# Performance work log

Hardware: AMD Instinct MI355X
Metric: run time of the kernel (lower is better)

## Reference

```python
import jax, jax.numpy as jnp
import numpy as np

EMBED = 1024
HEADS = 16
HEAD_DIM = EMBED // HEADS
OUT = 1024


def setup_inputs() -> dict:
    key = jax.random.key(0)
    ks = jax.random.split(key, 6)
    x = jax.random.normal(ks[0], (4, 2048, EMBED), dtype=jnp.float32)
    # per-head projection weights, torch Linear convention: [out_features, in_features]
    s = 1.0 / np.sqrt(HEAD_DIM)
    Wv = jax.random.uniform(ks[1], (HEAD_DIM, HEAD_DIM), jnp.float32, -s, s)
    Wk = jax.random.uniform(ks[2], (HEAD_DIM, HEAD_DIM), jnp.float32, -s, s)
    Wq = jax.random.uniform(ks[3], (HEAD_DIM, HEAD_DIM), jnp.float32, -s, s)
    so = 1.0 / np.sqrt(EMBED)
    Wo = jax.random.uniform(ks[4], (OUT, EMBED), jnp.float32, -so, so)
    bo = jax.random.uniform(ks[5], (OUT,), jnp.float32, -so, so)
    return {"x": x, "Wq": Wq, "Wk": Wk, "Wv": Wv, "Wo": Wo, "bo": bo}


def reference(x, Wq, Wk, Wv, Wo, bo):
    N, L, _ = x.shape
    xh = x.reshape(N, L, HEADS, HEAD_DIM)  # nqhd
    q = jnp.einsum('nqhd,ed->nqhe', xh, Wq)
    k = jnp.einsum('nkhd,ed->nkhe', xh, Wk)
    v = jnp.einsum('nkhd,ed->nkhe', xh, Wv)
    # full score matrix [N, H, Q, K], scaled by sqrt(embed_size) as in source
    energy = jnp.einsum('nqhd,nkhd->nhqk', q, k) / np.sqrt(EMBED).astype(np.float32)
    attn = jax.nn.softmax(energy, axis=3)
    out = jnp.einsum('nhqk,nkhd->nqhd', attn, v).reshape(N, L, EMBED)
    return out @ Wo.T + bo
```

## Files before the change

kernel.cpp:

```cpp
#include <hip/hip_runtime.h>
#include <hip/hip_bf16.h>
#include <stdint.h>
#include <stddef.h>


typedef __attribute__((ext_vector_type(8))) short bf16x8;
typedef __attribute__((ext_vector_type(4))) float f32x4;
typedef __attribute__((ext_vector_type(4))) short short4v;
typedef __attribute__((ext_vector_type(2))) uint32_t uint2v;

__device__ __forceinline__ f32x4 mfma16(bf16x8 a, bf16x8 b, f32x4 c) {
    return __builtin_amdgcn_mfma_f32_16x16x32_bf16(a, b, c, 0, 0, 0);
}

__device__ __forceinline__ short f2bf(float x) {
    union { float f; uint32_t u; } v; v.f = x;
    uint32_t r = (v.u + 0x7FFFu + ((v.u >> 16) & 1u)) >> 16;
    return (short)(uint16_t)r;
}

__device__ __forceinline__ uint32_t pk2bf(float a, float b) {
    union { __hip_bfloat162 h; uint32_t u; } v;
    v.h = __float22bfloat162_rn(float2{a, b});
    return v.u;
}

__device__ __forceinline__ bf16x8 cvt8(const float* __restrict__ p) {
    f32x4 a = *(const f32x4*)p;
    f32x4 b = *(const f32x4*)(p + 4);
    bf16x8 r;
    r[0] = f2bf(a[0]); r[1] = f2bf(a[1]); r[2] = f2bf(a[2]); r[3] = f2bf(a[3]);
    r[4] = f2bf(b[0]); r[5] = f2bf(b[1]); r[6] = f2bf(b[2]); r[7] = f2bf(b[3]);
    return r;
}

__device__ __forceinline__ void swap16(uint32_t a, uint32_t b,
                                       uint32_t& lo, uint32_t& hi) {
#if __has_builtin(__builtin_amdgcn_permlane16_swap)
    uint2v r = __builtin_amdgcn_permlane16_swap(a, b, false, false);
    lo = r[0]; hi = r[1];
#else
    int lane = (int)(threadIdx.x & 63);
    uint32_t bl = (uint32_t)__shfl((int)b, lane & 47);
    uint32_t ah = (uint32_t)__shfl((int)a, lane | 16);
    lo = (lane & 16) ? bl : a;
    hi = (lane & 16) ? b : ah;
#endif
}

__global__ __launch_bounds__(256)
void wpack_kernel(const float* __restrict__ Wo, const float* __restrict__ Wq,
                  const float* __restrict__ Wk, const float* __restrict__ Wv,
                  short* __restrict__ wo_f, short* __restrict__ wqkv_f) {
    int b = blockIdx.x;
    if (b < 512) {
        int idx = b * 256 + threadIdx.x;
        int nrow = idx >> 7;
        int k0 = (idx & 127) * 8;
        bf16x8 v = cvt8(Wo + (size_t)nrow * 1024 + k0);
        int ntile = nrow >> 4, lcn = nrow & 15;
        int kseg = k0 >> 5, qd = (k0 >> 3) & 3;
        *(bf16x8*)(wo_f + ((size_t)(ntile * 32 + kseg) * 64 + qd * 16 + lcn) * 8) = v;
    } else {
        const float* W = (b == 512) ? Wq : (b == 513) ? Wk : Wv;
        short* dst = wqkv_f + (size_t)(b - 512) * 4096;
        for (int u = threadIdx.x; u < 512; u += 256) {
            int seg = u >> 6, ln = u & 63;
            int nt = seg >> 1, kf = seg & 1, lq = ln >> 4, lcn = ln & 15;
            bf16x8 v = cvt8(W + (nt * 16 + lcn) * 64 + kf * 32 + lq * 8);
            *(bf16x8*)(dst + u * 8) = v;
        }
    }
}

__global__ __launch_bounds__(256)
void kvproj_kernel(const float* __restrict__ x, const short* __restrict__ wqkv_f,
                   short* __restrict__ kf_ws, short* __restrict__ vf_ws) {
    __shared__ alignas(16) short kbuf[128 * 72];
    __shared__ alignas(16) short vbuf[64 * 136];
    int tid = threadIdx.x;
    int lt = blockIdx.x & 15, nh = blockIdx.x >> 4;
    int n = nh >> 4, h = nh & 15;
    int l0 = lt * 128, kt0 = lt * 2;
    int wv = tid >> 6, lane = tid & 63, quad = lane >> 4, lc = lane & 15;
    const short* wkf = wqkv_f + 4096 + lane * 8;
    const short* wvf = wqkv_f + 8192 + lane * 8;

    for (int u = tid; u < 1024; u += 256) {
        int r = u >> 3, c = (u & 7) * 8;
        *(bf16x8*)(kbuf + r * 72 + c) =
            cvt8(x + (size_t)(n * 2048 + l0 + r) * 1024 + h * 64 + c);
    }
    __syncthreads();

    bf16x8 xa[2][2];
    for (int mt = 0; mt < 2; ++mt)
        for (int kf = 0; kf < 2; ++kf)
            xa[mt][kf] = *(bf16x8*)(kbuf + (wv * 32 + mt * 16 + lc) * 72 + kf * 32 + quad * 8);

    f32x4 ka[2][4] = {}, va[2][4] = {};
    for (int nt = 0; nt < 4; ++nt)
        for (int kf = 0; kf < 2; ++kf) {
            bf16x8 wkb = *(const bf16x8*)(wkf + (nt * 2 + kf) * 512);
            bf16x8 wvb = *(const bf16x8*)(wvf + (nt * 2 + kf) * 512);
            for (int mt = 0; mt < 2; ++mt) {
                ka[mt][nt] = mfma16(xa[mt][kf], wkb, ka[mt][nt]);
                va[mt][nt] = mfma16(xa[mt][kf], wvb, va[mt][nt]);
            }
        }

    for (int mt = 0; mt < 2; ++mt) {
        int off = wv * 32 + mt * 16;
        for (int nt = 0; nt < 4; ++nt) {
            short4v pv;
            for (int i = 0; i < 4; ++i) {
                kbuf[(off + quad * 4 + i) * 72 + nt * 16 + lc] = f2bf(ka[mt][nt][i]);
                pv[i] = f2bf(va[mt][nt][i]);
            }
            *(short4v*)(vbuf + (nt * 16 + lc) * 136 + off + quad * 4) = pv;
        }
    }
    __syncthreads();

    size_t base = (size_t)nh * 131072 + (size_t)kt0 * 4096;
    for (int u = tid; u < 1024; u += 256) {
        int tile = u >> 9, rem = u & 511, seg = rem >> 6, ln = u & 63;
        int t = seg >> 1, kf = seg & 1;
        int lq = ln >> 4, ll = ln & 15;
        int bq = ((lq & 1) << 1) | (lq >> 1);
        bf16x8 kw = *(bf16x8*)(kbuf + (tile * 64 + t * 16 + ll) * 72 + kf * 32 + lq * 8);
        *(bf16x8*)(kf_ws + base + (size_t)tile * 4096 + seg * 512 + ln * 8) = kw;
        bf16x8 vw = *(bf16x8*)(vbuf + (t * 16 + ll) * 136 + tile * 64 + kf * 32 + bq * 8);
        *(bf16x8*)(vf_ws + base + (size_t)tile * 4096 + seg * 512 + ln * 8) = vw;
    }
}

__global__ __launch_bounds__(256, 2)
void flash_kernel(const float* __restrict__ x, const short* __restrict__ wqkv_f,
                  const short* __restrict__ kf_ws, const short* __restrict__ vf_ws,
                  short* __restrict__ ao) {
    __shared__ alignas(16) short pbuf[256 * 72];
    int tid = threadIdx.x;
    int nh = blockIdx.x & 63, qt = blockIdx.x >> 6;
    int n = nh >> 4, h = nh & 15;
    int q0 = qt * 256;
    int wv = tid >> 6, lane = tid & 63, quad = lane >> 4, lc = lane & 15;

    for (int u = tid; u < 2048; u += 256) {
        int r = u >> 3, c = (u & 7) * 8;
        *(bf16x8*)(pbuf + r * 72 + c) =
            cvt8(x + (size_t)(n * 2048 + q0 + r) * 1024 + h * 64 + c);
    }
    __syncthreads();
    {
        const short* wqf = wqkv_f + lane * 8;
        bf16x8 xa[4][2];
        for (int mt = 0; mt < 4; ++mt)
            for (int kf = 0; kf < 2; ++kf)
                xa[mt][kf] = *(bf16x8*)(pbuf + (wv * 64 + mt * 16 + lc) * 72 +
                                        kf * 32 + quad * 8);
        f32x4 qacc[4][4] = {};
        for (int nt = 0; nt < 4; ++nt)
            for (int kf = 0; kf < 2; ++kf) {
                bf16x8 wb = *(const bf16x8*)(wqf + (nt * 2 + kf) * 512);
                for (int mt = 0; mt < 4; ++mt)
                    qacc[mt][nt] = mfma16(xa[mt][kf], wb, qacc[mt][nt]);
            }
        const float QS = 0.04508422002778011f;
        for (int mt = 0; mt < 4; ++mt)
            for (int nt = 0; nt < 4; ++nt)
                for (int i = 0; i < 4; ++i)
                    pbuf[(wv * 64 + mt * 16 + quad * 4 + i) * 72 + nt * 16 + lc] =
                        f2bf(qacc[mt][nt][i] * QS);
    }
    __syncthreads();
    bf16x8 qa[4][2];
    for (int mt = 0; mt < 4; ++mt)
        for (int kf = 0; kf < 2; ++kf)
            qa[mt][kf] = *(bf16x8*)(pbuf + (wv * 64 + mt * 16 + lc) * 72 +
                                    kf * 32 + quad * 8);

    f32x4 o[4][4] = {};
    float lsum[4] = {0.f, 0.f, 0.f, 0.f};
    const short* kbase = kf_ws + (size_t)nh * 131072 + lane * 8;
    const short* vbase = vf_ws + (size_t)nh * 131072 + lane * 8;

    for (int kt = 0; kt < 32; ++kt) {
        const short* kp = kbase + (size_t)kt * 4096;
        const short* vp = vbase + (size_t)kt * 4096;
        bf16x8 kA[4][2], vA[4][2];
#pragma unroll
        for (int t = 0; t < 4; ++t)
            for (int kf = 0; kf < 2; ++kf) {
                kA[t][kf] = *(const bf16x8*)(kp + (t * 2 + kf) * 512);
                vA[t][kf] = *(const bf16x8*)(vp + (t * 2 + kf) * 512);
            }

#pragma unroll
        for (int q2 = 0; q2 < 4; ++q2) {
            f32x4 s[4];
#pragma unroll
            for (int t = 0; t < 4; ++t) {
                f32x4 acc = {};
                acc = mfma16(kA[t][0], qa[q2][0], acc);
                acc = mfma16(kA[t][1], qa[q2][1], acc);
                s[t] = acc;
            }
            uint32_t p0[4], p1[4];
            float ts = 0.f;
#pragma unroll
            for (int t = 0; t < 4; ++t) {
                float e0 = __builtin_amdgcn_exp2f(s[t][0]);
                float e1 = __builtin_amdgcn_exp2f(s[t][1]);
                float e2 = __builtin_amdgcn_exp2f(s[t][2]);
                float e3 = __builtin_amdgcn_exp2f(s[t][3]);
                ts += (e0 + e1) + (e2 + e3);
                p0[t] = pk2bf(e0, e1);
                p1[t] = pk2bf(e2, e3);
            }
            lsum[q2] += ts;
#pragma unroll
            for (int kf = 0; kf < 2; ++kf) {
                uint32_t r0, r1, r2, r3;
                swap16(p0[2 * kf], p0[2 * kf + 1], r0, r2);
                swap16(p1[2 * kf], p1[2 * kf + 1], r1, r3);
                union { uint32_t u[4]; bf16x8 v; } fr;
                fr.u[0] = r0; fr.u[1] = r1; fr.u[2] = r2; fr.u[3] = r3;
#pragma unroll
                for (int dt = 0; dt < 4; ++dt)
                    o[q2][dt] = mfma16(vA[dt][kf], fr.v, o[q2][dt]);
            }
        }
    }

    for (int q2 = 0; q2 < 4; ++q2) {
        float t = lsum[q2];
        t += __shfl_xor(t, 16, 64);
        t += __shfl_xor(t, 32, 64);
        float inv = 1.f / t;
        int mtile = (n * 2048 + q0) / 16 + wv * 4 + q2;
        for (int dt = 0; dt < 4; ++dt) {
            int kseg = h * 2 + (dt >> 1);
            int qd8 = ((dt & 1) * 4 + quad) >> 1;
            short4v pk;
            for (int i = 0; i < 4; ++i) pk[i] = f2bf(o[q2][dt][i] * inv);
            *(short4v*)(ao + (size_t)(mtile * 32 + kseg) * 512 +
                        (qd8 * 16 + lc) * 8 + (quad & 1) * 4) = pk;
        }
    }
}

__global__ __launch_bounds__(256)
void outgemm_kernel(const short* __restrict__ afb, const short* __restrict__ wfb,
                    const float* __restrict__ bo, float* __restrict__ out) {
    int tid = threadIdx.x;
    int bm = blockIdx.x & 63, bn = blockIdx.x >> 6;
    int m0 = bm * 128, n0 = bn * 128;
    int wv = tid >> 6, lane = tid & 63, quad = lane >> 4, lc = lane & 15;
    int wr = wv >> 1, wc = wv & 1;
    int mtb = bm * 8 + wr * 4;
    int ntb = bn * 8 + wc * 4;

    const short* ab = afb + lane * 8;
    const short* bb = wfb + lane * 8;

    f32x4 acc[4][4] = {};
    for (int kt = 0; kt < 32; ++kt) {
        bf16x8 af[4], bfr[4];
#pragma unroll
        for (int mt = 0; mt < 4; ++mt)
            af[mt] = *(const bf16x8*)(ab + ((size_t)(mtb + mt) * 32 + kt) * 512);
#pragma unroll
        for (int nt = 0; nt < 4; ++nt)
            bfr[nt] = *(const bf16x8*)(bb + ((size_t)(ntb + nt) * 32 + kt) * 512);
#pragma unroll
        for (int mt = 0; mt < 4; ++mt)
            for (int nt = 0; nt < 4; ++nt)
                acc[mt][nt] = mfma16(af[mt], bfr[nt], acc[mt][nt]);
    }
    for (int nt = 0; nt < 4; ++nt) {
        float bv = bo[n0 + wc * 64 + nt * 16 + lc];
        for (int mt = 0; mt < 4; ++mt)
            for (int i = 0; i < 4; ++i) {
                int m = m0 + wr * 64 + mt * 16 + quad * 4 + i;
                int nn = n0 + wc * 64 + nt * 16 + lc;
                out[(size_t)m * 1024 + nn] = acc[mt][nt][i] + bv;
            }
    }
}

extern "C" void kernel_launch(void* const* d_in, const int* in_sizes, int n_in,
                              void* d_out, int out_size, void* d_ws, size_t ws_size,
                              hipStream_t stream) {
    const float* x  = (const float*)d_in[0];
    const float* Wq = (const float*)d_in[1];
    const float* Wk = (const float*)d_in[2];
    const float* Wv = (const float*)d_in[3];
    const float* Wo = (const float*)d_in[4];
    const float* bo = (const float*)d_in[5];
    float* out = (float*)d_out;

    short* kf_ws   = (short*)d_ws;
    short* vf_ws   = kf_ws + 8388608;
    short* ao_ws   = vf_ws + 8388608;
    short* wo_f    = ao_ws + 8388608;
    short* wqkv_f  = wo_f + 1048576;

    wpack_kernel<<<dim3(515), dim3(256), 0, stream>>>(Wo, Wq, Wk, Wv, wo_f, wqkv_f);
    kvproj_kernel<<<dim3(1024), dim3(256), 0, stream>>>(x, wqkv_f, kf_ws, vf_ws);
    flash_kernel<<<dim3(512), dim3(256), 0, stream>>>(x, wqkv_f, kf_ws, vf_ws, ao_ws);
    outgemm_kernel<<<dim3(512), dim3(256), 0, stream>>>(ao_ws, wo_f, bo, out);
}
```

Before: 203.3 us.

## Software-pipeline K tile prefetch and pair query tiles with setprio in attention loop

Restructures the attention inner loop to double-buffer K fragments, prefetching the next tile's K while the current tile is processed. V for each tile is loaded just before use. Query sub-tiles are processed in pairs so two score blocks are in flight, and s_setprio raises wave priority around the MFMA phases. The aim is to hide global load latency and interleave exp/softmax work with matrix ops, at the cost of more live registers and possible occupancy loss.

```diff
diff --git a/kernel.cpp b/kernel.cpp
--- a/kernel.cpp
+++ b/kernel.cpp
@@ -185,52 +185,79 @@
     const short* kbase = kf_ws + (size_t)nh * 131072 + lane * 8;
     const short* vbase = vf_ws + (size_t)nh * 131072 + lane * 8;
 
-    for (int kt = 0; kt < 32; ++kt) {
-        const short* kp = kbase + (size_t)kt * 4096;
+    bf16x8 kR[4][2], kS[4][2], vR[4][2];
+
+    auto LOADK = [&](bf16x8 (&dst)[4][2], int kt) {
+        const short* kp = kbase + (size_t)(kt & 31) * 4096;
+#pragma unroll
+        for (int t = 0; t < 4; ++t)
+            for (int kf = 0; kf < 2; ++kf)
+                dst[t][kf] = *(const bf16x8*)(kp + (t * 2 + kf) * 512);
+    };
+    auto LOADV = [&](bf16x8 (&dst)[4][2], int kt) {
         const short* vp = vbase + (size_t)kt * 4096;
-        bf16x8 kA[4][2], vA[4][2];
 #pragma unroll
         for (int t = 0; t < 4; ++t)
-            for (int kf = 0; kf < 2; ++kf) {
-                kA[t][kf] = *(const bf16x8*)(kp + (t * 2 + kf) * 512);
-                vA[t][kf] = *(const bf16x8*)(vp + (t * 2 + kf) * 512);
-            }
-
-#pragma unroll
-        for (int q2 = 0; q2 < 4; ++q2) {
-            f32x4 s[4];
-#pragma unroll
-            for (int t = 0; t < 4; ++t) {
-                f32x4 acc = {};
-                acc = mfma16(kA[t][0], qa[q2][0], acc);
-                acc = mfma16(kA[t][1], qa[q2][1], acc);
-                s[t] = acc;
-            }
-            uint32_t p0[4], p1[4];
-            float ts = 0.f;
-#pragma unroll
-            for (int t = 0; t < 4; ++t) {
-                float e0 = __builtin_amdgcn_exp2f(s[t][0]);
-                float e1 = __builtin_amdgcn_exp2f(s[t][1]);
-                float e2 = __builtin_amdgcn_exp2f(s[t][2]);
-                float e3 = __builtin_amdgcn_exp2f(s[t][3]);
-                ts += (e0 + e1) + (e2 + e3);
-                p0[t] = pk2bf(e0, e1);
-                p1[t] = pk2bf(e2, e3);
-            }
-            lsum[q2] += ts;
-#pragma unroll
-            for (int kf = 0; kf < 2; ++kf) {
-                uint32_t r0, r1, r2, r3;
-                swap16(p0[2 * kf], p0[2 * kf + 1], r0, r2);
-                swap16(p1[2 * kf], p1[2 * kf + 1], r1, r3);
-                union { uint32_t u[4]; bf16x8 v; } fr;
-                fr.u[0] = r0; fr.u[1] = r1; fr.u[2] = r2; fr.u[3] = r3;
-#pragma unroll
-                for (int dt = 0; dt < 4; ++dt)
-                    o[q2][dt] = mfma16(vA[dt][kf], fr.v, o[q2][dt]);
-            }
-        }
+            for (int kf = 0; kf < 2; ++kf)
+                dst[t][kf] = *(const bf16x8*)(vp + (t * 2 + kf) * 512);
+    };
+
+    auto BODY = [&](bf16x8 (&kA)[4][2], bf16x8 (&vA)[4][2]) {
+#pragma unroll
+        for (int qp = 0; qp < 2; ++qp) {
+            f32x4 s[2][4];
+            __builtin_amdgcn_s_setprio(1);
+#pragma unroll
+            for (int q = 0; q < 2; ++q)
+                for (int t = 0; t < 4; ++t) {
+                    f32x4 acc = {};
+                    acc = mfma16(kA[t][0], qa[qp * 2 + q][0], acc);
+                    acc = mfma16(kA[t][1], qa[qp * 2 + q][1], acc);
+                    s[q][t] = acc;
+                }
+            __builtin_amdgcn_s_setprio(0);
+            uint32_t P0[2][4], P1[2][4];
+#pragma unroll
+            for (int q = 0; q < 2; ++q) {
+                float ts = 0.f;
+#pragma unroll
+                for (int t = 0; t < 4; ++t) {
+                    float e0 = __builtin_amdgcn_exp2f(s[q][t][0]);
+                    float e1 = __builtin_amdgcn_exp2f(s[q][t][1]);
+                    float e2 = __builtin_amdgcn_exp2f(s[q][t][2]);
+                    float e3 = __builtin_amdgcn_exp2f(s[q][t][3]);
+                    ts += (e0 + e1) + (e2 + e3);
+                    P0[q][t] = pk2bf(e0, e1);
+                    P1[q][t] = pk2bf(e2, e3);
+                }
+                lsum[qp * 2 + q] += ts;
+            }
+            __builtin_amdgcn_s_setprio(1);
+#pragma unroll
+            for (int q = 0; q < 2; ++q)
+                for (int kf = 0; kf < 2; ++kf) {
+                    uint32_t r0, r1, r2, r3;
+                    swap16(P0[q][2 * kf], P0[q][2 * kf + 1], r0, r2);
+                    swap16(P1[q][2 * kf], P1[q][2 * kf + 1], r1, r3);
+                    union { uint32_t u[4]; bf16x8 v; } fr;
+                    fr.u[0] = r0; fr.u[1] = r1; fr.u[2] = r2; fr.u[3] = r3;
+#pragma unroll
+                    for (int dt = 0; dt < 4; ++dt)
+                        o[qp * 2 + q][dt] =
+                            mfma16(vA[dt][kf], fr.v, o[qp * 2 + q][dt]);
+                }
+            __builtin_amdgcn_s_setprio(0);
+        }
+    };
+
+    LOADK(kR, 0);
+    for (int kt = 0; kt < 32; kt += 2) {
+        LOADV(vR, kt);
+        LOADK(kS, kt + 1);
+        BODY(kR, vR);
+        LOADV(vR, kt + 1);
+        LOADK(kR, (kt + 2) & 31);
+        BODY(kS, vR);
     }
 
     for (int q2 = 0; q2 < 4; ++q2) {
```

Measured after the change: 367.2 us. 1.81x slower.

## Software-pipeline K/V fragment loads with inline asm and manual vmcnt waits

Applied to the files above, without the earlier changes.

Replaces the per-iteration combined K and V loads with a double-staged scheme. K for the next tile is prefetched via inline global_load_dwordx4 while V for the current tile is in flight, and explicit s_waitcnt vmcnt(8) waits hold each fragment set until it has arrived. The QK/softmax phase for all four query subtiles now runs before the PV phase, so all P fragments are held in registers at once. This is meant to hide global load latency behind MFMA work. The cost is higher register pressure, and correctness depends on the fixed vmcnt counting. The last iteration also issues a wasted wraparound K load.

```diff
diff --git a/kernel.cpp b/kernel.cpp
--- a/kernel.cpp
+++ b/kernel.cpp
@@ -33,6 +33,15 @@
     r[4] = f2bf(b[0]); r[5] = f2bf(b[1]); r[6] = f2bf(b[2]); r[7] = f2bf(b[3]);
     return r;
 }
+
+#define GLOAD(dst, src) \
+    asm volatile("global_load_dwordx4 %0, %1, off" : "=v"(dst) : "v"(src))
+
+#define WAITFRAGS(B)                                                        \
+    asm volatile("s_waitcnt vmcnt(8)"                                       \
+                 : "+v"(B[0][0]), "+v"(B[0][1]), "+v"(B[1][0]),             \
+                   "+v"(B[1][1]), "+v"(B[2][0]), "+v"(B[2][1]),             \
+                   "+v"(B[3][0]), "+v"(B[3][1]))
 
 __device__ __forceinline__ void swap16(uint32_t a, uint32_t b,
                                        uint32_t& lo, uint32_t& hi) {
@@ -185,17 +194,25 @@
     const short* kbase = kf_ws + (size_t)nh * 131072 + lane * 8;
     const short* vbase = vf_ws + (size_t)nh * 131072 + lane * 8;
 
+    bf16x8 kA[4][2], vA[4][2];
+
+#pragma unroll
+    for (int t = 0; t < 4; ++t)
+        for (int kf = 0; kf < 2; ++kf)
+            GLOAD(kA[t][kf], kbase + (t * 2 + kf) * 512);
+
     for (int kt = 0; kt < 32; ++kt) {
-        const short* kp = kbase + (size_t)kt * 4096;
         const short* vp = vbase + (size_t)kt * 4096;
-        bf16x8 kA[4][2], vA[4][2];
+        const short* kp = kbase + (size_t)((kt + 1) & 31) * 4096;
+
 #pragma unroll
         for (int t = 0; t < 4; ++t)
-            for (int kf = 0; kf < 2; ++kf) {
-                kA[t][kf] = *(const bf16x8*)(kp + (t * 2 + kf) * 512);
-                vA[t][kf] = *(const bf16x8*)(vp + (t * 2 + kf) * 512);
-            }
-
+            for (int kf = 0; kf < 2; ++kf)
+                GLOAD(vA[t][kf], vp + (t * 2 + kf) * 512);
+
+        WAITFRAGS(kA);
+
+        uint32_t p0[4][4], p1[4][4];
 #pragma unroll
         for (int q2 = 0; q2 < 4; ++q2) {
             f32x4 s[4];
@@ -206,7 +223,6 @@
                 acc = mfma16(kA[t][1], qa[q2][1], acc);
                 s[t] = acc;
             }
-            uint32_t p0[4], p1[4];
             float ts = 0.f;
 #pragma unroll
             for (int t = 0; t < 4; ++t) {
@@ -215,22 +231,31 @@
                 float e2 = __builtin_amdgcn_exp2f(s[t][2]);
                 float e3 = __builtin_amdgcn_exp2f(s[t][3]);
                 ts += (e0 + e1) + (e2 + e3);
-                p0[t] = pk2bf(e0, e1);
-                p1[t] = pk2bf(e2, e3);
+                p0[q2][t] = pk2bf(e0, e1);
+                p1[q2][t] = pk2bf(e2, e3);
             }
             lsum[q2] += ts;
-#pragma unroll
+        }
+
+#pragma unroll
+        for (int t = 0; t < 4; ++t)
+            for (int kf = 0; kf < 2; ++kf)
+                GLOAD(kA[t][kf], kp + (t * 2 + kf) * 512);
+
+        WAITFRAGS(vA);
+
+#pragma unroll
+        for (int q2 = 0; q2 < 4; ++q2)
             for (int kf = 0; kf < 2; ++kf) {
                 uint32_t r0, r1, r2, r3;
-                swap16(p0[2 * kf], p0[2 * kf + 1], r0, r2);
-                swap16(p1[2 * kf], p1[2 * kf + 1], r1, r3);
+                swap16(p0[q2][2 * kf], p0[q2][2 * kf + 1], r0, r2);
+                swap16(p1[q2][2 * kf], p1[q2][2 * kf + 1], r1, r3);
                 union { uint32_t u[4]; bf16x8 v; } fr;
                 fr.u[0] = r0; fr.u[1] = r1; fr.u[2] = r2; fr.u[3] = r3;
 #pragma unroll
                 for (int dt = 0; dt < 4; ++dt)
                     o[q2][dt] = mfma16(vA[dt][kf], fr.v, o[q2][dt]);
             }
-        }
     }
 
     for (int q2 = 0; q2 < 4; ++q2) {
```

Measured after the change: 196.2 us. 3.5% less time.
